# Performance work log

Hardware: AMD Instinct MI355X
Metric: run time of the kernel (lower is better)

Reference implementation:

```python
import jax, jax.numpy as jnp
import numpy as np

N_NODES = 50000
N_EDGES = 800000
N_GLOBALS = 64
DX, DE, DU = 128, 32, 32
HID, OUT = 128, 128
EPS = 1e-5


def _mlp(x, W1, b1, W2, b2, g, b):
    # Linear -> ReLU -> Linear -> ReLU (activate_final) -> LayerNorm (normalize)
    h = jax.nn.relu(x @ W1 + b1)
    h = jax.nn.relu(h @ W2 + b2)
    mu = jnp.mean(h, axis=-1, keepdims=True)
    var = jnp.var(h, axis=-1, keepdims=True)
    return g * (h - mu) * jax.lax.rsqrt(var + EPS) + b


def _mlp_params(key, d_in):
    k1, k2 = jax.random.split(key)
    W1 = jax.random.normal(k1, (d_in, HID), jnp.float32) / np.sqrt(d_in)
    b1 = jnp.zeros((HID,), jnp.float32)
    W2 = jax.random.normal(k2, (HID, OUT), jnp.float32) / np.sqrt(HID)
    b2 = jnp.zeros((OUT,), jnp.float32)
    g = jnp.ones((OUT,), jnp.float32)
    b = jnp.zeros((OUT,), jnp.float32)
    return W1, b1, W2, b2, g, b


def setup_inputs() -> dict:
    key = jax.random.key(0)
    ks = jax.random.split(key, 8)
    x = jax.random.normal(ks[0], (N_NODES, DX), jnp.float32)
    e = jax.random.normal(ks[1], (N_EDGES, DE), jnp.float32)
    u = jax.random.normal(ks[2], (N_GLOBALS, DU), jnp.float32)
    edge_index = jax.random.randint(ks[3], (2, N_EDGES), 0, N_NODES, jnp.int64 if jax.config.jax_enable_x64 else jnp.int32)
    batch = jnp.sort(jax.random.randint(ks[4], (N_NODES,), 0, N_GLOBALS))
    # edge MLP in: e(32) + recv(128) + send(128) + u(32) = 320
    eW1, eb1, eW2, eb2, eg, ebt = _mlp_params(ks[5], DE + DX + DX + DU)
    # node MLP in: x(128) + edge_aggr(128) + u(32) = 288
    nW1, nb1, nW2, nb2, ng, nbt = _mlp_params(ks[6], DX + OUT + DU)
    # global MLP in: u(32) + node_aggr(128) + edge_aggr(128) = 288
    gW1, gb1, gW2, gb2, gg, gbt = _mlp_params(ks[7], DU + OUT + OUT)
    return dict(x=x, e=e, u=u, edge_index=edge_index, batch=batch,
                eW1=eW1, eb1=eb1, eW2=eW2, eb2=eb2, eg=eg, ebt=ebt,
                nW1=nW1, nb1=nb1, nW2=nW2, nb2=nb2, ng=ng, nbt=nbt,
                gW1=gW1, gb1=gb1, gW2=gW2, gb2=gb2, gg=gg, gbt=gbt)


def reference(x, e, u, edge_index, batch,
              eW1, eb1, eW2, eb2, eg, ebt,
              nW1, nb1, nW2, nb2, ng, nbt,
              gW1, gb1, gW2, gb2, gg, gbt):
    row, col = edge_index[0], edge_index[1]
    edge_batch = batch[row]  # graph id per edge

    # --- EdgeModel: concat(edge, receiver, sender, global->edges) -> MLP ---
    edge_in = jnp.concatenate([e, x[col], x[row], u[edge_batch]], axis=1)
    e2 = _mlp(edge_in, eW1, eb1, eW2, eb2, eg, ebt)  # [N_EDGES, OUT]

    # --- NodeModel: concat(node, edges->node via receiver, global->nodes) -> MLP ---
    edge_to_node = jax.ops.segment_sum(e2, col, num_segments=N_NODES)
    node_in = jnp.concatenate([x, edge_to_node, u[batch]], axis=1)
    x2 = _mlp(node_in, nW1, nb1, nW2, nb2, ng, nbt)  # [N_NODES, OUT]

    # --- GlobalModel: concat(global, nodes->global, edges->global) -> MLP ---
    node_to_glob = jax.ops.segment_sum(x2, batch, num_segments=N_GLOBALS)
    edge_to_glob = jax.ops.segment_sum(e2, edge_batch, num_segments=N_GLOBALS)
    glob_in = jnp.concatenate([u, node_to_glob, edge_to_glob], axis=1)
    u2 = _mlp(glob_in, gW1, gb1, gW2, gb2, gg, gbt)  # [N_GLOBALS, OUT]

    return x2, e2, u2
```

## Files before the change

### kernel.cpp

```cpp
#include <hip/hip_runtime.h>
#include <hip/hip_bf16.h>

typedef __attribute__((ext_vector_type(8))) short bf16x8;
typedef __attribute__((ext_vector_type(4))) float f32x4;

#define EPSV 1e-5f
#define NN 50000
#define NE 800000
#define NG 64
#define SEGB 1000
#define MFMA16(a, b, c) __builtin_amdgcn_mfma_f32_16x16x32_bf16(a, b, c, 0, 0, 0)

__device__ __forceinline__ unsigned short f2bf(float f) {
  union { float f; unsigned u; } v; v.f = f;
  unsigned r = v.u + 0x7FFFu + ((v.u >> 16) & 1u);
  return (unsigned short)(r >> 16);
}
__device__ __forceinline__ float bf2f(unsigned short h) {
  union { unsigned u; float f; } v; v.u = ((unsigned)h) << 16;
  return v.f;
}


__global__ __launch_bounds__(256) void cvt_vec_kernel(
    const float* __restrict__ x, unsigned short* __restrict__ xb) {
  const int NX4 = (NN * 128) / 4;
  for (int idx = blockIdx.x * 256 + threadIdx.x; idx < NX4;
       idx += gridDim.x * 256) {
    float4 v = ((const float4*)x)[idx];
    ushort4 o;
    o.x = f2bf(v.x); o.y = f2bf(v.y); o.z = f2bf(v.z); o.w = f2bf(v.w);
    ((ushort4*)xb)[idx] = o;
  }
}

__global__ __launch_bounds__(256) void cvt_small_kernel(
    const float* __restrict__ u,
    const float* __restrict__ eW1, const float* __restrict__ eW2,
    const float* __restrict__ nW1, const float* __restrict__ nW2,
    unsigned short* __restrict__ ub,
    unsigned short* __restrict__ W1eT, unsigned short* __restrict__ WpqT,
    unsigned short* __restrict__ eW2T,
    unsigned short* __restrict__ nW1T, unsigned short* __restrict__ nW2T,
    float* __restrict__ Rg) {
  int i = blockIdx.x * 256 + threadIdx.x;
  const int R0 = NG * 32;
  const int R1 = R0 + 128 * 32;
  const int R2 = R1 + 256 * 128;
  const int R3 = R2 + 128 * 128;
  const int R4 = R3 + 128 * 320;
  const int R5 = R4 + 128 * 128;
  const int R6 = R5 + NG * 128;
  if (i < R0) {
    ub[i] = f2bf(u[i]);
  } else if (i < R1) {
    int j = i - R0; int n = j >> 5, k = j & 31;
    W1eT[j] = f2bf(eW1[k * 128 + n]);
  } else if (i < R2) {
    int j = i - R1; int n = j >> 7, k = j & 127;
    WpqT[j] = (n < 128) ? f2bf(eW1[(32 + k) * 128 + n])
                        : f2bf(eW1[(160 + k) * 128 + (n - 128)]);
  } else if (i < R3) {
    int j = i - R2; int n = j >> 7, k = j & 127;
    eW2T[j] = f2bf(eW2[k * 128 + n]);
  } else if (i < R4) {
    int j = i - R3; int n = j / 320, k = j % 320;
    nW1T[j] = (k < 288) ? f2bf(nW1[k * 128 + n]) : (unsigned short)0;
  } else if (i < R5) {
    int j = i - R4; int n = j >> 7, k = j & 127;
    nW2T[j] = f2bf(nW2[k * 128 + n]);
  } else if (i < R6) {
    int j = i - R5; int g = j >> 7, n = j & 127;
    float s = 0.f;
#pragma unroll
    for (int k = 0; k < 32; ++k) s += u[g * 32 + k] * eW1[(288 + k) * 128 + n];
    Rg[j] = s;
  }
}

__global__ __launch_bounds__(256, 2) void pq_kernel(
    const unsigned short* __restrict__ xb,
    const unsigned short* __restrict__ WpqT,
    unsigned short* __restrict__ PQ) {
  __shared__ __align__(16) unsigned short Asm[64][136];
  __shared__ __align__(16) unsigned short Bsm[256][72];
  const int tid = threadIdx.x;
  {
    const int r = tid >> 2, q = tid & 3;
    const int grow = blockIdx.x * 64 + r;
    const uint4 zero = {0u, 0u, 0u, 0u};
    if (grow < NN) {
      const uint4* xs = (const uint4*)(xb + (size_t)grow * 128 + q * 32);
#pragma unroll
      for (int k = 0; k < 4; ++k) *(uint4*)&Asm[r][q * 32 + k * 8] = xs[k];
    } else {
#pragma unroll
      for (int k = 0; k < 4; ++k) *(uint4*)&Asm[r][q * 32 + k * 8] = zero;
    }
  }
  const int w = tid >> 6, lane = tid & 63;
  const int l15 = lane & 15, lg = lane >> 4;
  f32x4 acc[16];
#pragma unroll
  for (int ni = 0; ni < 16; ++ni) acc[ni] = f32x4{0.f, 0.f, 0.f, 0.f};
  for (int kc = 0; kc < 2; ++kc) {
    {
      const uint4* src = (const uint4*)(WpqT + (size_t)tid * 128 + kc * 64);
#pragma unroll
      for (int k = 0; k < 8; ++k) *(uint4*)&Bsm[tid][k * 8] = src[k];
    }
    __syncthreads();
    bf16x8 a0 = *(bf16x8*)&Asm[w * 16 + l15][kc * 64 + lg * 8];
    bf16x8 a1 = *(bf16x8*)&Asm[w * 16 + l15][kc * 64 + 32 + lg * 8];
#pragma unroll
    for (int ni = 0; ni < 16; ++ni) {
      bf16x8 b0 = *(bf16x8*)&Bsm[ni * 16 + l15][lg * 8];
      bf16x8 b1 = *(bf16x8*)&Bsm[ni * 16 + l15][32 + lg * 8];
      acc[ni] = MFMA16(a0, b0, acc[ni]);
      acc[ni] = MFMA16(a1, b1, acc[ni]);
    }
    __syncthreads();
  }
  unsigned short (*Cl)[264] = (unsigned short(*)[264])&Bsm[0][0];
#pragma unroll
  for (int ni = 0; ni < 16; ++ni)
#pragma unroll
    for (int reg = 0; reg < 4; ++reg)
      Cl[w * 16 + lg * 4 + reg][l15 + ni * 16] = f2bf(acc[ni][reg]);
  __syncthreads();
  {
    const int r = tid >> 2, q = tid & 3;
    const int grow = blockIdx.x * 64 + r;
    if (grow < NN) {
#pragma unroll
      for (int k = 0; k < 8; ++k)
        *(uint4*)(PQ + (size_t)grow * 256 + q * 64 + k * 8) =
            *(uint4*)&Cl[r][q * 64 + k * 8];
    }
  }
}


__global__ __launch_bounds__(256) void pre_kernel(
    const int* __restrict__ rowIdx, const int* __restrict__ colIdx,
    int* __restrict__ cnt_r, int* __restrict__ cnt_s) {
  int i = blockIdx.x * 256 + threadIdx.x;
  if (i < NE) {
    atomicAdd(&cnt_r[colIdx[i]], 1);
    atomicAdd(&cnt_s[rowIdx[i]], 1);
  }
}

__global__ __launch_bounds__(1024) void scan2_kernel(
    const int* __restrict__ cnt_r, int* __restrict__ offs_r, int* __restrict__ cur_r,
    const int* __restrict__ cnt_s, int* __restrict__ offs_s, int* __restrict__ cur_s) {
  __shared__ int sums[1024];
  const int* cnt = blockIdx.x ? cnt_s : cnt_r;
  int* offs = blockIdx.x ? offs_s : offs_r;
  int* cur  = blockIdx.x ? cur_s : cur_r;
  const int t = threadIdx.x;
  const int base = t * 49;
  int s = 0;
  for (int j = 0; j < 49; ++j) {
    int idx = base + j;
    if (idx < NN) s += cnt[idx];
  }
  sums[t] = s;
  __syncthreads();
  for (int off = 1; off < 1024; off <<= 1) {
    int add = (t >= off) ? sums[t - off] : 0;
    __syncthreads();
    sums[t] += add;
    __syncthreads();
  }
  int run = (t == 0) ? 0 : sums[t - 1];
  for (int j = 0; j < 49; ++j) {
    int idx = base + j;
    if (idx < NN) {
      offs[idx] = run; cur[idx] = run;
      run += cnt[idx];
    }
  }
}

__global__ __launch_bounds__(256) void fill_both_kernel(
    const int* __restrict__ rowIdx, const int* __restrict__ colIdx,
    const int* __restrict__ batch,
    int* __restrict__ cur_r, int* __restrict__ cur_s,
    int* __restrict__ eidlist_r, int* __restrict__ eidlist_s,
    int* __restrict__ gs) {
  int i = blockIdx.x * 256 + threadIdx.x;
  if (i < NE) {
    const int c = colIdx[i];
    const int p = atomicAdd(&cur_r[c], 1);
    eidlist_r[p] = i;
    const int r = rowIdx[i];
    const int p2 = atomicAdd(&cur_s[r], 1);
    eidlist_s[p2] = i;
    gs[p2] = batch[r];
  }
}

__global__ __launch_bounds__(256, 3) void edge_kernel(
    const float* __restrict__ ef,
    const unsigned short* __restrict__ PQ,
    const float* __restrict__ Rg,
    const int* __restrict__ rowI, const int* __restrict__ colI,
    const int* __restrict__ batch,
    const unsigned short* __restrict__ W1eT,
    const unsigned short* __restrict__ W2T,
    const float* __restrict__ b1, const float* __restrict__ b2,
    const float* __restrict__ gam, const float* __restrict__ bet,
    float* __restrict__ outE) {
  __shared__ __align__(16) char U[27648];
  __shared__ __align__(16) unsigned short Hsm[64][136];
  __shared__ float cb1[128], cb2[128], cg[128], cbt[128];
  unsigned short (*B1e)[40] = (unsigned short(*)[40])U;
  unsigned short (*Ssm)[136] = (unsigned short(*)[136])(U + 10240);
  unsigned short (*Bsm)[72] = (unsigned short(*)[72])U;

  const int tid = threadIdx.x;
  const int base = blockIdx.x * 64;
  if (tid < 128) {
    cb1[tid] = b1[tid]; cb2[tid] = b2[tid];
    cg[tid] = gam[tid]; cbt[tid] = bet[tid];
    const uint4* s = (const uint4*)(W1eT + tid * 32);
#pragma unroll
    for (int k = 0; k < 4; ++k) *(uint4*)&B1e[tid][k * 8] = s[k];
  }

  {
    const int r = tid >> 2, q = tid & 3;
    const int grow = base + r;
    const int rcv = colI[grow];
    const int snd = rowI[grow];
    const int g = batch[snd];
    const unsigned short* pp = PQ + (size_t)rcv * 256 + q * 32;
    const unsigned short* qq = PQ + (size_t)snd * 256 + 128 + q * 32;
    const float* rr = Rg + g * 128 + q * 32;
#pragma unroll
    for (int k = 0; k < 8; ++k) {
      ushort4 pv = *(const ushort4*)(pp + k * 4);
      ushort4 qv = *(const ushort4*)(qq + k * 4);
      float4 rv = *(const float4*)(rr + k * 4);
      ushort4 o;
      o.x = f2bf(bf2f(pv.x) + bf2f(qv.x) + rv.x);
      o.y = f2bf(bf2f(pv.y) + bf2f(qv.y) + rv.y);
      o.z = f2bf(bf2f(pv.z) + bf2f(qv.z) + rv.z);
      o.w = f2bf(bf2f(pv.w) + bf2f(qv.w) + rv.w);
      *(ushort4*)&Ssm[r][q * 32 + k * 4] = o;
    }
  }
  __syncthreads();

  const int w = tid >> 6, lane = tid & 63;
  const int l15 = lane & 15, lg = lane >> 4;

  f32x4 acc[8];
#pragma unroll
  for (int ni = 0; ni < 8; ++ni) acc[ni] = f32x4{0.f, 0.f, 0.f, 0.f};
  {
    const int arow = base + w * 16 + l15;
    const float* ep = ef + (size_t)arow * 32 + lg * 8;
    float4 v0 = *(const float4*)ep;
    float4 v1 = *(const float4*)(ep + 4);
    bf16x8 a;
    a[0] = (short)f2bf(v0.x); a[1] = (short)f2bf(v0.y);
    a[2] = (short)f2bf(v0.z); a[3] = (short)f2bf(v0.w);
    a[4] = (short)f2bf(v1.x); a[5] = (short)f2bf(v1.y);
    a[6] = (short)f2bf(v1.z); a[7] = (short)f2bf(v1.w);
#pragma unroll
    for (int ni = 0; ni < 8; ++ni) {
      bf16x8 b0 = *(bf16x8*)&B1e[ni * 16 + l15][lg * 8];
      acc[ni] = MFMA16(a, b0, acc[ni]);
    }
  }

#pragma unroll
  for (int ni = 0; ni < 8; ++ni) {
    const int ncol = l15 + ni * 16;
    const float bias = cb1[ncol];
#pragma unroll
    for (int reg = 0; reg < 4; ++reg) {
      const int mrow = w * 16 + lg * 4 + reg;
      const float sv = bf2f(Ssm[mrow][ncol]);
      Hsm[mrow][ncol] = f2bf(fmaxf(acc[ni][reg] + sv + bias, 0.f));
    }
  }
  __syncthreads();

  f32x4 acc2[8];
#pragma unroll
  for (int ni = 0; ni < 8; ++ni) acc2[ni] = f32x4{0.f, 0.f, 0.f, 0.f};
  for (int kc = 0; kc < 2; ++kc) {
    {
      const int n = tid >> 1, half = tid & 1;
      const uint4* src = (const uint4*)(W2T + (size_t)n * 128 + kc * 64 + half * 32);
#pragma unroll
      for (int k = 0; k < 4; ++k)
        *(uint4*)&Bsm[n][half * 32 + k * 8] = src[k];
    }
    __syncthreads();
    bf16x8 a0 = *(bf16x8*)&Hsm[w * 16 + l15][kc * 64 + lg * 8];
    bf16x8 a1 = *(bf16x8*)&Hsm[w * 16 + l15][kc * 64 + 32 + lg * 8];
#pragma unroll
    for (int ni = 0; ni < 8; ++ni) {
      bf16x8 b0 = *(bf16x8*)&Bsm[ni * 16 + l15][lg * 8];
      bf16x8 b1 = *(bf16x8*)&Bsm[ni * 16 + l15][32 + lg * 8];
      acc2[ni] = MFMA16(a0, b0, acc2[ni]);
      acc2[ni] = MFMA16(a1, b1, acc2[ni]);
    }
    __syncthreads();
  }

  float hv[8][4];
  float sreg[4] = {0.f, 0.f, 0.f, 0.f}, ssreg[4] = {0.f, 0.f, 0.f, 0.f};
#pragma unroll
  for (int ni = 0; ni < 8; ++ni) {
    const int ncol = l15 + ni * 16;
    const float bias = cb2[ncol];
#pragma unroll
    for (int reg = 0; reg < 4; ++reg) {
      const float h = fmaxf(acc2[ni][reg] + bias, 0.f);
      hv[ni][reg] = h;
      sreg[reg] += h; ssreg[reg] += h * h;
    }
  }
#pragma unroll
  for (int reg = 0; reg < 4; ++reg) {
    float s = sreg[reg], ss = ssreg[reg];
#pragma unroll
    for (int off = 1; off < 16; off <<= 1) {
      s += __shfl_xor(s, off, 64);
      ss += __shfl_xor(ss, off, 64);
    }
    sreg[reg] = s; ssreg[reg] = ss;
  }
#pragma unroll
  for (int reg = 0; reg < 4; ++reg) {
    const int grow = base + w * 16 + lg * 4 + reg;
    const float mu = sreg[reg] * (1.f / 128.f);
    const float var = ssreg[reg] * (1.f / 128.f) - mu * mu;
    const float rstd = rsqrtf(var + EPSV);
#pragma unroll
    for (int ni = 0; ni < 8; ++ni) {
      const int ncol = l15 + ni * 16;
      const float y = cg[ncol] * (hv[ni][reg] - mu) * rstd + cbt[ncol];
      outE[(size_t)grow * 128 + ncol] = y;
    }
  }
}

__global__ __launch_bounds__(256, 3) void post_kernel(
    const float* __restrict__ outE,
    const int* __restrict__ eidl_s, const int* __restrict__ gsA,
    float* __restrict__ e2g,
    const unsigned short* __restrict__ xb,
    const unsigned short* __restrict__ ub,
    const int* __restrict__ batch,
    const int* __restrict__ offs, const int* __restrict__ cnt,
    const int* __restrict__ eidlist,
    const unsigned short* __restrict__ W1T,
    const unsigned short* __restrict__ W2T,
    const float* __restrict__ b1, const float* __restrict__ b2,
    const float* __restrict__ gam, const float* __restrict__ bet,
    float* __restrict__ outX, float* __restrict__ n2g) {
  __shared__ __align__(16) char U[33792];
  __shared__ __align__(16) unsigned short Usm[64][40];
  __shared__ __align__(16) unsigned short Bsm[128][40];
  __shared__ float cb1[128], cb2[128], cg[128], cbt[128];

  const int tid = threadIdx.x;

  if (blockIdx.x < SEGB) {
    const int c4 = (tid & 31) * 4;
    const int sub = tid >> 5;
    const int start = blockIdx.x * 800;
    int gcur = gsA[start + sub];
    float4 acc = {0.f, 0.f, 0.f, 0.f};
    for (int it = 0; it < 25; ++it) {
      const int pbase = start + sub + it * 32;
      int eid[4], g[4];
#pragma unroll
      for (int j = 0; j < 4; ++j) {
        eid[j] = eidl_s[pbase + j * 8];
        g[j]   = gsA[pbase + j * 8];
      }
      float4 v[4];
#pragma unroll
      for (int j = 0; j < 4; ++j)
        v[j] = *(const float4*)(outE + (size_t)eid[j] * 128 + c4);
#pragma unroll
      for (int j = 0; j < 4; ++j) {
        if (g[j] != gcur) {
          atomicAdd(&e2g[gcur * 128 + c4],     acc.x);
          atomicAdd(&e2g[gcur * 128 + c4 + 1], acc.y);
          atomicAdd(&e2g[gcur * 128 + c4 + 2], acc.z);
          atomicAdd(&e2g[gcur * 128 + c4 + 3], acc.w);
          gcur = g[j]; acc = float4{0.f, 0.f, 0.f, 0.f};
        }
        acc.x += v[j].x; acc.y += v[j].y; acc.z += v[j].z; acc.w += v[j].w;
      }
    }
    atomicAdd(&e2g[gcur * 128 + c4],     acc.x);
    atomicAdd(&e2g[gcur * 128 + c4 + 1], acc.y);
    atomicAdd(&e2g[gcur * 128 + c4 + 2], acc.z);
    atomicAdd(&e2g[gcur * 128 + c4 + 3], acc.w);
    return;
  }

  const int bx = blockIdx.x - SEGB;
  unsigned short (*Asm)[264] = (unsigned short(*)[264])U;
  unsigned short (*Hsm)[136] = (unsigned short(*)[136])U;
  float* bins = (float*)(U + 17408);

  if (tid < 128) {
    cb1[tid] = b1[tid]; cb2[tid] = b2[tid];
    cg[tid] = gam[tid]; cbt[tid] = bet[tid];
  }

  const int gmin = batch[bx * 64];
  const int gmax = batch[min(bx * 64 + 63, NN - 1)];
  const bool fastbins = (gmax - gmin) < 8;

  {
    const int r = tid >> 2, q = tid & 3;
    const int grow = bx * 64 + r;
    const bool valid = grow < NN;
    const uint4 zero = {0u, 0u, 0u, 0u};
    if (valid) {
      const uint4* xs = (const uint4*)(xb + (size_t)grow * 128 + q * 32);
#pragma unroll
      for (int k = 0; k < 4; ++k) *(uint4*)&Asm[r][q * 32 + k * 8] = xs[k];
    } else {
#pragma unroll
      for (int k = 0; k < 4; ++k) *(uint4*)&Asm[r][q * 32 + k * 8] = zero;
    }
    float4 a[8];
#pragma unroll
    for (int k = 0; k < 8; ++k) a[k] = float4{0.f, 0.f, 0.f, 0.f};
    if (valid) {
      const int start = offs[grow];
      const int deg = cnt[grow];
      int j = 0;
      for (; j + 2 <= deg; j += 2) {
        const int e0 = eidlist[start + j], e1 = eidlist[start + j + 1];
        const float4* s0 = (const float4*)(outE + (size_t)e0 * 128 + q * 32);
        const float4* s1 = (const float4*)(outE + (size_t)e1 * 128 + q * 32);
#pragma unroll
        for (int k = 0; k < 8; ++k) {
          float4 v0 = s0[k], v1 = s1[k];
          a[k].x += v0.x + v1.x; a[k].y += v0.y + v1.y;
          a[k].z += v0.z + v1.z; a[k].w += v0.w + v1.w;
        }
      }
      if (j < deg) {
        const int e0 = eidlist[start + j];
        const float4* s0 = (const float4*)(outE + (size_t)e0 * 128 + q * 32);
#pragma unroll
        for (int k = 0; k < 8; ++k) {
          float4 v0 = s0[k];
          a[k].x += v0.x; a[k].y += v0.y; a[k].z += v0.z; a[k].w += v0.w;
        }
      }
    }
#pragma unroll
    for (int k = 0; k < 8; ++k) {
      ushort4 o;
      o.x = f2bf(a[k].x); o.y = f2bf(a[k].y);
      o.z = f2bf(a[k].z); o.w = f2bf(a[k].w);
      *(ushort4*)&Asm[r][128 + q * 32 + k * 4] = o;
    }
    const int g = valid ? batch[grow] : 0;
    uint4 uv = valid ? *(const uint4*)(ub + g * 32 + q * 8) : zero;
    *(uint4*)&Usm[r][q * 8] = uv;
  }

  const int w = tid >> 6;
  const int lane = tid & 63;
  const int l15 = lane & 15, lg = lane >> 4;

  f32x4 acc[8];
#pragma unroll
  for (int ni = 0; ni < 8; ++ni) acc[ni] = f32x4{0.f, 0.f, 0.f, 0.f};

  for (int kc = 0; kc < 9; ++kc) {
    {
      const int n = tid >> 1, half = tid & 1;
      const uint4* src = (const uint4*)(W1T + (size_t)n * 320 + kc * 32 + half * 16);
      *(uint4*)&Bsm[n][half * 16] = src[0];
      *(uint4*)&Bsm[n][half * 16 + 8] = src[1];
    }
    __syncthreads();
    bf16x8 a0 = (kc < 8) ? *(bf16x8*)&Asm[w * 16 + l15][kc * 32 + lg * 8]
                         : *(bf16x8*)&Usm[w * 16 + l15][lg * 8];
#pragma unroll
    for (int ni = 0; ni < 8; ++ni) {
      bf16x8 bb = *(bf16x8*)&Bsm[ni * 16 + l15][lg * 8];
      acc[ni] = MFMA16(a0, bb, acc[ni]);
    }
    __syncthreads();
  }

#pragma unroll
  for (int ni = 0; ni < 8; ++ni) {
    const int ncol = l15 + ni * 16;
    const float bias = cb1[ncol];
#pragma unroll
    for (int reg = 0; reg < 4; ++reg) {
      const int mrow = w * 16 + lg * 4 + reg;
      Hsm[mrow][ncol] = f2bf(fmaxf(acc[ni][reg] + bias, 0.f));
    }
  }
  for (int i = tid; i < 8 * 128; i += 256) bins[i] = 0.f;

  f32x4 acc2[8];
#pragma unroll
  for (int ni = 0; ni < 8; ++ni) acc2[ni] = f32x4{0.f, 0.f, 0.f, 0.f};
  for (int kc = 0; kc < 4; ++kc) {
    {
      const int n = tid >> 1, half = tid & 1;
      const uint4* src = (const uint4*)(W2T + (size_t)n * 128 + kc * 32 + half * 16);
      *(uint4*)&Bsm[n][half * 16] = src[0];
      *(uint4*)&Bsm[n][half * 16 + 8] = src[1];
    }
    __syncthreads();
    bf16x8 a0 = *(bf16x8*)&Hsm[w * 16 + l15][kc * 32 + lg * 8];
#pragma unroll
    for (int ni = 0; ni < 8; ++ni) {
      bf16x8 bb = *(bf16x8*)&Bsm[ni * 16 + l15][lg * 8];
      acc2[ni] = MFMA16(a0, bb, acc2[ni]);
    }
    __syncthreads();
  }

  float hv[8][4];
  float sreg[4] = {0.f, 0.f, 0.f, 0.f}, ssreg[4] = {0.f, 0.f, 0.f, 0.f};
#pragma unroll
  for (int ni = 0; ni < 8; ++ni) {
    const int ncol = l15 + ni * 16;
    const float bias = cb2[ncol];
#pragma unroll
    for (int reg = 0; reg < 4; ++reg) {
      const float h = fmaxf(acc2[ni][reg] + bias, 0.f);
      hv[ni][reg] = h;
      sreg[reg] += h; ssreg[reg] += h * h;
    }
  }
#pragma unroll
  for (int reg = 0; reg < 4; ++reg) {
    float s = sreg[reg], ss = ssreg[reg];
#pragma unroll
    for (int off = 1; off < 16; off <<= 1) {
      s += __shfl_xor(s, off, 64);
      ss += __shfl_xor(ss, off, 64);
    }
    sreg[reg] = s; ssreg[reg] = ss;
  }
#pragma unroll
  for (int reg = 0; reg < 4; ++reg) {
    const int mrow = w * 16 + lg * 4 + reg;
    const int grow = bx * 64 + mrow;
    if (grow >= NN) continue;
    const float mu = sreg[reg] * (1.f / 128.f);
    const float var = ssreg[reg] * (1.f / 128.f) - mu * mu;
    const float rstd = rsqrtf(var + EPSV);
    const int g = batch[grow];
#pragma unroll
    for (int ni = 0; ni < 8; ++ni) {
      const int ncol = l15 + ni * 16;
      const float y = cg[ncol] * (hv[ni][reg] - mu) * rstd + cbt[ncol];
      outX[(size_t)grow * 128 + ncol] = y;
      if (fastbins) atomicAdd(&bins[(g - gmin) * 128 + ncol], y);
      else          atomicAdd(&n2g[g * 128 + ncol], y);
    }
  }
  if (fastbins) {
    __syncthreads();
    const int cntf = (gmax - gmin + 1) * 128;
    for (int i = tid; i < cntf; i += 256)
      atomicAdd(&n2g[gmin * 128 + i], bins[i]);
  }
}

__global__ __launch_bounds__(128) void glob_kernel(
    const float* __restrict__ u, const float* __restrict__ n2g,
    const float* __restrict__ e2g,
    const float* __restrict__ gW1, const float* __restrict__ gb1,
    const float* __restrict__ gW2, const float* __restrict__ gb2,
    const float* __restrict__ gg, const float* __restrict__ gbt,
    float* __restrict__ outU) {
  __shared__ float in[288];
  __shared__ float h1[128];
  __shared__ float red[4];
  const int g = blockIdx.x, t = threadIdx.x;
  if (t < 32) in[t] = u[g * 32 + t];
  in[32 + t] = n2g[g * 128 + t];
  in[160 + t] = e2g[g * 128 + t];
  __syncthreads();
  float a = gb1[t];
  for (int k = 0; k < 288; ++k) a += in[k] * gW1[k * 128 + t];
  h1[t] = fmaxf(a, 0.f);
  __syncthreads();
  float h = gb2[t];
  for (int k = 0; k < 128; ++k) h += h1[k] * gW2[k * 128 + t];
  h = fmaxf(h, 0.f);
  float s = h, ss = h * h;
  for (int off = 1; off < 64; off <<= 1) {
    s += __shfl_xor(s, off, 64);
    ss += __shfl_xor(ss, off, 64);
  }
  if ((t & 63) == 0) { red[(t >> 6) * 2] = s; red[(t >> 6) * 2 + 1] = ss; }
  __syncthreads();
  const float S = red[0] + red[2], SS = red[1] + red[3];
  const float mu = S * (1.f / 128.f);
  const float var = SS * (1.f / 128.f) - mu * mu;
  const float rstd = rsqrtf(var + EPSV);
  outU[g * 128 + t] = gg[t] * (h - mu) * rstd + gbt[t];
}

extern "C" void kernel_launch(void* const* d_in, const int* in_sizes, int n_in,
                              void* d_out, int out_size, void* d_ws,
                              size_t ws_size, hipStream_t stream) {
  const float* x   = (const float*)d_in[0];
  const float* e   = (const float*)d_in[1];
  const float* u   = (const float*)d_in[2];
  const int* eidx  = (const int*)d_in[3];
  const int* batch = (const int*)d_in[4];
  const float* eW1 = (const float*)d_in[5];
  const float* eb1 = (const float*)d_in[6];
  const float* eW2 = (const float*)d_in[7];
  const float* eb2 = (const float*)d_in[8];
  const float* eg  = (const float*)d_in[9];
  const float* ebt = (const float*)d_in[10];
  const float* nW1 = (const float*)d_in[11];
  const float* nb1 = (const float*)d_in[12];
  const float* nW2 = (const float*)d_in[13];
  const float* nb2 = (const float*)d_in[14];
  const float* ng  = (const float*)d_in[15];
  const float* nbt = (const float*)d_in[16];
  const float* gW1 = (const float*)d_in[17];
  const float* gb1 = (const float*)d_in[18];
  const float* gW2 = (const float*)d_in[19];
  const float* gb2 = (const float*)d_in[20];
  const float* gg  = (const float*)d_in[21];
  const float* gbt = (const float*)d_in[22];

  char* ws = (char*)d_ws;
  float* e2g           = (float*)(ws + 0);
  float* n2g           = (float*)(ws + 32768);
  int*   cnt_r         = (int*)  (ws + 65536);
  int*   cnt_s         = (int*)  (ws + 265536);
  int*   offs_r        = (int*)  (ws + 465536);
  int*   cur_r         = (int*)  (ws + 665536);
  int*   offs_s        = (int*)  (ws + 865536);
  int*   cur_s         = (int*)  (ws + 1065536);
  int*   eidlist_r     = (int*)  (ws + 1265536);
  int*   eidlist_s     = (int*)  (ws + 4465536);
  int*   gs            = (int*)  (ws + 7665536);
  unsigned short* xb   = (unsigned short*)(ws + 10865536);
  unsigned short* ub   = (unsigned short*)(ws + 23665536);
  unsigned short* W1eT = (unsigned short*)(ws + 23669632);
  unsigned short* WpqT = (unsigned short*)(ws + 23677824);
  unsigned short* eW2T = (unsigned short*)(ws + 23743360);
  unsigned short* nW1T = (unsigned short*)(ws + 23776128);
  unsigned short* nW2T = (unsigned short*)(ws + 23858048);
  unsigned short* PQ   = (unsigned short*)(ws + 23890816);
  float* Rg            = (float*)(ws + 49490816);

  hipMemsetAsync(ws, 0, 465536, stream);

  cvt_vec_kernel<<<1024, 256, 0, stream>>>(x, xb);
  cvt_small_kernel<<<472, 256, 0, stream>>>(u, eW1, eW2, nW1, nW2, ub, W1eT,
                                            WpqT, eW2T, nW1T, nW2T, Rg);
  pq_kernel<<<(NN + 63) / 64, 256, 0, stream>>>(xb, WpqT, PQ);

  float* outX = (float*)d_out;
  float* outE = outX + (size_t)NN * 128;
  float* outU = outE + (size_t)NE * 128;

  const int* rowI = eidx;
  const int* colI = eidx + NE;

  pre_kernel<<<(NE + 255) / 256, 256, 0, stream>>>(rowI, colI, cnt_r, cnt_s);
  scan2_kernel<<<2, 1024, 0, stream>>>(cnt_r, offs_r, cur_r,
                                       cnt_s, offs_s, cur_s);
  fill_both_kernel<<<(NE + 255) / 256, 256, 0, stream>>>(
      rowI, colI, batch, cur_r, cur_s, eidlist_r, eidlist_s, gs);

  edge_kernel<<<NE / 64, 256, 0, stream>>>(e, PQ, Rg, rowI, colI, batch,
                                           W1eT, eW2T, eb1, eb2, eg, ebt,
                                           outE);
  post_kernel<<<SEGB + (NN + 63) / 64, 256, 0, stream>>>(
      outE, eidlist_s, gs, e2g,
      xb, ub, batch, offs_r, cnt_r, eidlist_r,
      nW1T, nW2T, nb1, nb2, ng, nbt, outX, n2g);
  glob_kernel<<<NG, 128, 0, stream>>>(u, n2g, e2g, gW1, gb1, gW2, gb2, gg, gbt,
                                      outU);
}
```

Before: 842.4 us.

## Fuse edge-to-global segment sum into persistent edge kernel via shared-memory bins

Makes the edge kernel persistent over 512 blocks and accumulates each edge output row into per-block LDS bins indexed by graph id. The bins are written as per-block partials and summed by a small reduction kernel. This removes the sender-sorted CSR build (counting, scan and fill for senders) and the separate pass that re-read all of outE for the global aggregation. The cost is 128 LDS atomics per edge row, 32 KB of extra shared memory that lowers occupancy to 2 blocks per CU, and a 16 MB partial buffer plus its reduction.

```diff
diff --git a/kernel.cpp b/kernel.cpp
--- a/kernel.cpp
+++ b/kernel.cpp
@@ -8,7 +8,7 @@
 #define NN 50000
 #define NE 800000
 #define NG 64
-#define SEGB 1000
+#define EGRID 512
 #define MFMA16(a, b, c) __builtin_amdgcn_mfma_f32_16x16x32_bf16(a, b, c, 0, 0, 0)
 
 __device__ __forceinline__ unsigned short f2bf(float f) {
@@ -142,22 +142,15 @@
 
 
 __global__ __launch_bounds__(256) void pre_kernel(
-    const int* __restrict__ rowIdx, const int* __restrict__ colIdx,
-    int* __restrict__ cnt_r, int* __restrict__ cnt_s) {
+    const int* __restrict__ colIdx, int* __restrict__ cnt_r) {
   int i = blockIdx.x * 256 + threadIdx.x;
-  if (i < NE) {
-    atomicAdd(&cnt_r[colIdx[i]], 1);
-    atomicAdd(&cnt_s[rowIdx[i]], 1);
-  }
-}
-
-__global__ __launch_bounds__(1024) void scan2_kernel(
-    const int* __restrict__ cnt_r, int* __restrict__ offs_r, int* __restrict__ cur_r,
-    const int* __restrict__ cnt_s, int* __restrict__ offs_s, int* __restrict__ cur_s) {
+  if (i < NE) atomicAdd(&cnt_r[colIdx[i]], 1);
+}
+
+__global__ __launch_bounds__(1024) void scan_kernel(
+    const int* __restrict__ cnt, int* __restrict__ offs,
+    int* __restrict__ cur) {
   __shared__ int sums[1024];
-  const int* cnt = blockIdx.x ? cnt_s : cnt_r;
-  int* offs = blockIdx.x ? offs_s : offs_r;
-  int* cur  = blockIdx.x ? cur_s : cur_r;
   const int t = threadIdx.x;
   const int base = t * 49;
   int s = 0;
@@ -183,25 +176,17 @@
   }
 }
 
-__global__ __launch_bounds__(256) void fill_both_kernel(
-    const int* __restrict__ rowIdx, const int* __restrict__ colIdx,
-    const int* __restrict__ batch,
-    int* __restrict__ cur_r, int* __restrict__ cur_s,
-    int* __restrict__ eidlist_r, int* __restrict__ eidlist_s,
-    int* __restrict__ gs) {
+__global__ __launch_bounds__(256) void fill_kernel(
+    const int* __restrict__ colIdx, int* __restrict__ cur,
+    int* __restrict__ eidlist) {
   int i = blockIdx.x * 256 + threadIdx.x;
   if (i < NE) {
-    const int c = colIdx[i];
-    const int p = atomicAdd(&cur_r[c], 1);
-    eidlist_r[p] = i;
-    const int r = rowIdx[i];
-    const int p2 = atomicAdd(&cur_s[r], 1);
-    eidlist_s[p2] = i;
-    gs[p2] = batch[r];
-  }
-}
-
-__global__ __launch_bounds__(256, 3) void edge_kernel(
+    int p = atomicAdd(&cur[colIdx[i]], 1);
+    eidlist[p] = i;
+  }
+}
+
+__global__ __launch_bounds__(256, 2) void edge_kernel(
     const float* __restrict__ ef,
     const unsigned short* __restrict__ PQ,
     const float* __restrict__ Rg,
@@ -211,16 +196,15 @@
     const unsigned short* __restrict__ W2T,
     const float* __restrict__ b1, const float* __restrict__ b2,
     const float* __restrict__ gam, const float* __restrict__ bet,
-    float* __restrict__ outE) {
-  __shared__ __align__(16) char U[27648];
-  __shared__ __align__(16) unsigned short Hsm[64][136];
+    float* __restrict__ outE, float* __restrict__ e2g_part) {
+  __shared__ __align__(16) unsigned short B1e[128][40];
+  __shared__ __align__(16) unsigned short SH[64][136];
+  __shared__ __align__(16) unsigned short Bsm[128][72];
+  __shared__ float bins[NG * 128];
   __shared__ float cb1[128], cb2[128], cg[128], cbt[128];
-  unsigned short (*B1e)[40] = (unsigned short(*)[40])U;
-  unsigned short (*Ssm)[136] = (unsigned short(*)[136])(U + 10240);
-  unsigned short (*Bsm)[72] = (unsigned short(*)[72])U;
+  __shared__ int gsm[64];
 
   const int tid = threadIdx.x;
-  const int base = blockIdx.x * 64;
   if (tid < 128) {
     cb1[tid] = b1[tid]; cb2[tid] = b2[tid];
     cg[tid] = gam[tid]; cbt[tid] = bet[tid];
@@ -228,133 +212,153 @@
 #pragma unroll
     for (int k = 0; k < 4; ++k) *(uint4*)&B1e[tid][k * 8] = s[k];
   }
-
-  {
-    const int r = tid >> 2, q = tid & 3;
-    const int grow = base + r;
-    const int rcv = colI[grow];
-    const int snd = rowI[grow];
-    const int g = batch[snd];
-    const unsigned short* pp = PQ + (size_t)rcv * 256 + q * 32;
-    const unsigned short* qq = PQ + (size_t)snd * 256 + 128 + q * 32;
-    const float* rr = Rg + g * 128 + q * 32;
-#pragma unroll
-    for (int k = 0; k < 8; ++k) {
-      ushort4 pv = *(const ushort4*)(pp + k * 4);
-      ushort4 qv = *(const ushort4*)(qq + k * 4);
-      float4 rv = *(const float4*)(rr + k * 4);
-      ushort4 o;
-      o.x = f2bf(bf2f(pv.x) + bf2f(qv.x) + rv.x);
-      o.y = f2bf(bf2f(pv.y) + bf2f(qv.y) + rv.y);
-      o.z = f2bf(bf2f(pv.z) + bf2f(qv.z) + rv.z);
-      o.w = f2bf(bf2f(pv.w) + bf2f(qv.w) + rv.w);
-      *(ushort4*)&Ssm[r][q * 32 + k * 4] = o;
-    }
-  }
+  for (int i = tid; i < NG * 128; i += 256) bins[i] = 0.f;
   __syncthreads();
 
   const int w = tid >> 6, lane = tid & 63;
   const int l15 = lane & 15, lg = lane >> 4;
 
-  f32x4 acc[8];
-#pragma unroll
-  for (int ni = 0; ni < 8; ++ni) acc[ni] = f32x4{0.f, 0.f, 0.f, 0.f};
-  {
-    const int arow = base + w * 16 + l15;
-    const float* ep = ef + (size_t)arow * 32 + lg * 8;
-    float4 v0 = *(const float4*)ep;
-    float4 v1 = *(const float4*)(ep + 4);
-    bf16x8 a;
-    a[0] = (short)f2bf(v0.x); a[1] = (short)f2bf(v0.y);
-    a[2] = (short)f2bf(v0.z); a[3] = (short)f2bf(v0.w);
-    a[4] = (short)f2bf(v1.x); a[5] = (short)f2bf(v1.y);
-    a[6] = (short)f2bf(v1.z); a[7] = (short)f2bf(v1.w);
+  for (int tile = blockIdx.x; tile < NE / 64; tile += gridDim.x) {
+    const int base = tile * 64;
+
+    {
+      const int r = tid >> 2, q = tid & 3;
+      const int grow = base + r;
+      const int rcv = colI[grow];
+      const int snd = rowI[grow];
+      const int g = batch[snd];
+      if (q == 0) gsm[r] = g;
+      const unsigned short* pp = PQ + (size_t)rcv * 256 + q * 32;
+      const unsigned short* qq = PQ + (size_t)snd * 256 + 128 + q * 32;
+      const float* rr = Rg + g * 128 + q * 32;
+#pragma unroll
+      for (int k = 0; k < 8; ++k) {
+        ushort4 pv = *(const ushort4*)(pp + k * 4);
+        ushort4 qv = *(const ushort4*)(qq + k * 4);
+        float4 rv = *(const float4*)(rr + k * 4);
+        ushort4 o;
+        o.x = f2bf(bf2f(pv.x) + bf2f(qv.x) + rv.x);
+        o.y = f2bf(bf2f(pv.y) + bf2f(qv.y) + rv.y);
+        o.z = f2bf(bf2f(pv.z) + bf2f(qv.z) + rv.z);
+        o.w = f2bf(bf2f(pv.w) + bf2f(qv.w) + rv.w);
+        *(ushort4*)&SH[r][q * 32 + k * 4] = o;
+      }
+    }
+    __syncthreads();
+
+    f32x4 acc[8];
+#pragma unroll
+    for (int ni = 0; ni < 8; ++ni) acc[ni] = f32x4{0.f, 0.f, 0.f, 0.f};
+    {
+      const int arow = base + w * 16 + l15;
+      const float* ep = ef + (size_t)arow * 32 + lg * 8;
+      float4 v0 = *(const float4*)ep;
+      float4 v1 = *(const float4*)(ep + 4);
+      bf16x8 a;
+      a[0] = (short)f2bf(v0.x); a[1] = (short)f2bf(v0.y);
+      a[2] = (short)f2bf(v0.z); a[3] = (short)f2bf(v0.w);
+      a[4] = (short)f2bf(v1.x); a[5] = (short)f2bf(v1.y);
+      a[6] = (short)f2bf(v1.z); a[7] = (short)f2bf(v1.w);
+#pragma unroll
+      for (int ni = 0; ni < 8; ++ni) {
+        bf16x8 b0 = *(bf16x8*)&B1e[ni * 16 + l15][lg * 8];
+        acc[ni] = MFMA16(a, b0, acc[ni]);
+      }
+    }
+
 #pragma unroll
     for (int ni = 0; ni < 8; ++ni) {
-      bf16x8 b0 = *(bf16x8*)&B1e[ni * 16 + l15][lg * 8];
-      acc[ni] = MFMA16(a, b0, acc[ni]);
-    }
-  }
-
-#pragma unroll
-  for (int ni = 0; ni < 8; ++ni) {
-    const int ncol = l15 + ni * 16;
-    const float bias = cb1[ncol];
+      const int ncol = l15 + ni * 16;
+      const float bias = cb1[ncol];
+#pragma unroll
+      for (int reg = 0; reg < 4; ++reg) {
+        const int mrow = w * 16 + lg * 4 + reg;
+        const float sv = bf2f(SH[mrow][ncol]);
+        SH[mrow][ncol] = f2bf(fmaxf(acc[ni][reg] + sv + bias, 0.f));
+      }
+    }
+    __syncthreads();
+
+    f32x4 acc2[8];
+#pragma unroll
+    for (int ni = 0; ni < 8; ++ni) acc2[ni] = f32x4{0.f, 0.f, 0.f, 0.f};
+    for (int kc = 0; kc < 2; ++kc) {
+      {
+        const int n = tid >> 1, half = tid & 1;
+        const uint4* src = (const uint4*)(W2T + (size_t)n * 128 + kc * 64 + half * 32);
+#pragma unroll
+        for (int k = 0; k < 4; ++k)
+          *(uint4*)&Bsm[n][half * 32 + k * 8] = src[k];
+      }
+      __syncthreads();
+      bf16x8 a0 = *(bf16x8*)&SH[w * 16 + l15][kc * 64 + lg * 8];
+      bf16x8 a1 = *(bf16x8*)&SH[w * 16 + l15][kc * 64 + 32 + lg * 8];
+#pragma unroll
+      for (int ni = 0; ni < 8; ++ni) {
+        bf16x8 b0 = *(bf16x8*)&Bsm[ni * 16 + l15][lg * 8];
+        bf16x8 b1 = *(bf16x8*)&Bsm[ni * 16 + l15][32 + lg * 8];
+        acc2[ni] = MFMA16(a0, b0, acc2[ni]);
+        acc2[ni] = MFMA16(a1, b1, acc2[ni]);
+      }
+      __syncthreads();
+    }
+
+    float hv[8][4];
+    float sreg[4] = {0.f, 0.f, 0.f, 0.f}, ssreg[4] = {0.f, 0.f, 0.f, 0.f};
+#pragma unroll
+    for (int ni = 0; ni < 8; ++ni) {
+      const int ncol = l15 + ni * 16;
+      const float bias = cb2[ncol];
+#pragma unroll
+      for (int reg = 0; reg < 4; ++reg) {
+        const float h = fmaxf(acc2[ni][reg] + bias, 0.f);
+        hv[ni][reg] = h;
+        sreg[reg] += h; ssreg[reg] += h * h;
+      }
+    }
+#pragma unroll
+    for (int reg = 0; reg < 4; ++reg) {
+      float s = sreg[reg], ss = ssreg[reg];
+#pragma unroll
+      for (int off = 1; off < 16; off <<= 1) {
+        s += __shfl_xor(s, off, 64);
+        ss += __shfl_xor(ss, off, 64);
+      }
+      sreg[reg] = s; ssreg[reg] = ss;
+    }
 #pragma unroll
     for (int reg = 0; reg < 4; ++reg) {
       const int mrow = w * 16 + lg * 4 + reg;
-      const float sv = bf2f(Ssm[mrow][ncol]);
-      Hsm[mrow][ncol] = f2bf(fmaxf(acc[ni][reg] + sv + bias, 0.f));
-    }
-  }
-  __syncthreads();
-
-  f32x4 acc2[8];
-#pragma unroll
-  for (int ni = 0; ni < 8; ++ni) acc2[ni] = f32x4{0.f, 0.f, 0.f, 0.f};
-  for (int kc = 0; kc < 2; ++kc) {
-    {
-      const int n = tid >> 1, half = tid & 1;
-      const uint4* src = (const uint4*)(W2T + (size_t)n * 128 + kc * 64 + half * 32);
-#pragma unroll
-      for (int k = 0; k < 4; ++k)
-        *(uint4*)&Bsm[n][half * 32 + k * 8] = src[k];
-    }
-    __syncthreads();
-    bf16x8 a0 = *(bf16x8*)&Hsm[w * 16 + l15][kc * 64 + lg * 8];
-    bf16x8 a1 = *(bf16x8*)&Hsm[w * 16 + l15][kc * 64 + 32 + lg * 8];
-#pragma unroll
-    for (int ni = 0; ni < 8; ++ni) {
-      bf16x8 b0 = *(bf16x8*)&Bsm[ni * 16 + l15][lg * 8];
-      bf16x8 b1 = *(bf16x8*)&Bsm[ni * 16 + l15][32 + lg * 8];
-      acc2[ni] = MFMA16(a0, b0, acc2[ni]);
-      acc2[ni] = MFMA16(a1, b1, acc2[ni]);
-    }
-    __syncthreads();
-  }
-
-  float hv[8][4];
-  float sreg[4] = {0.f, 0.f, 0.f, 0.f}, ssreg[4] = {0.f, 0.f, 0.f, 0.f};
-#pragma unroll
-  for (int ni = 0; ni < 8; ++ni) {
-    const int ncol = l15 + ni * 16;
-    const float bias = cb2[ncol];
-#pragma unroll
-    for (int reg = 0; reg < 4; ++reg) {
-      const float h = fmaxf(acc2[ni][reg] + bias, 0.f);
-      hv[ni][reg] = h;
-      sreg[reg] += h; ssreg[reg] += h * h;
-    }
-  }
-#pragma unroll
-  for (int reg = 0; reg < 4; ++reg) {
-    float s = sreg[reg], ss = ssreg[reg];
-#pragma unroll
-    for (int off = 1; off < 16; off <<= 1) {
-      s += __shfl_xor(s, off, 64);
-      ss += __shfl_xor(ss, off, 64);
-    }
-    sreg[reg] = s; ssreg[reg] = ss;
-  }
-#pragma unroll
-  for (int reg = 0; reg < 4; ++reg) {
-    const int grow = base + w * 16 + lg * 4 + reg;
-    const float mu = sreg[reg] * (1.f / 128.f);
-    const float var = ssreg[reg] * (1.f / 128.f) - mu * mu;
-    const float rstd = rsqrtf(var + EPSV);
-#pragma unroll
-    for (int ni = 0; ni < 8; ++ni) {
-      const int ncol = l15 + ni * 16;
-      const float y = cg[ncol] * (hv[ni][reg] - mu) * rstd + cbt[ncol];
-      outE[(size_t)grow * 128 + ncol] = y;
-    }
-  }
-}
-
-__global__ __launch_bounds__(256, 3) void post_kernel(
+      const int grow = base + mrow;
+      const float mu = sreg[reg] * (1.f / 128.f);
+      const float var = ssreg[reg] * (1.f / 128.f) - mu * mu;
+      const float rstd = rsqrtf(var + EPSV);
+      const int gr = gsm[mrow];
+#pragma unroll
+      for (int ni = 0; ni < 8; ++ni) {
+        const int ncol = l15 + ni * 16;
+        const float y = cg[ncol] * (hv[ni][reg] - mu) * rstd + cbt[ncol];
+        outE[(size_t)grow * 128 + ncol] = y;
+        atomicAdd(&bins[gr * 128 + ncol], y);
+      }
+    }
+    __syncthreads();
+  }
+
+  float* dst = e2g_part + (size_t)blockIdx.x * (NG * 128);
+  for (int i = tid; i < NG * 128; i += 256) dst[i] = bins[i];
+}
+
+__global__ __launch_bounds__(256) void e2g_reduce_kernel(
+    const float* __restrict__ part, float* __restrict__ e2g) {
+  const int i = blockIdx.x * 256 + threadIdx.x;
+  float s = 0.f;
+  for (int p = 0; p < EGRID; ++p) s += part[(size_t)p * (NG * 128) + i];
+  e2g[i] = s;
+}
+
+__global__ __launch_bounds__(256, 3) void node_kernel(
     const float* __restrict__ outE,
-    const int* __restrict__ eidl_s, const int* __restrict__ gsA,
-    float* __restrict__ e2g,
     const unsigned short* __restrict__ xb,
     const unsigned short* __restrict__ ub,
     const int* __restrict__ batch,
@@ -371,45 +375,7 @@
   __shared__ float cb1[128], cb2[128], cg[128], cbt[128];
 
   const int tid = threadIdx.x;
-
-  if (blockIdx.x < SEGB) {
-    const int c4 = (tid & 31) * 4;
-    const int sub = tid >> 5;
-    const int start = blockIdx.x * 800;
-    int gcur = gsA[start + sub];
-    float4 acc = {0.f, 0.f, 0.f, 0.f};
-    for (int it = 0; it < 25; ++it) {
-      const int pbase = start + sub + it * 32;
-      int eid[4], g[4];
-#pragma unroll
-      for (int j = 0; j < 4; ++j) {
-        eid[j] = eidl_s[pbase + j * 8];
-        g[j]   = gsA[pbase + j * 8];
-      }
-      float4 v[4];
-#pragma unroll
-      for (int j = 0; j < 4; ++j)
-        v[j] = *(const float4*)(outE + (size_t)eid[j] * 128 + c4);
-#pragma unroll
-      for (int j = 0; j < 4; ++j) {
-        if (g[j] != gcur) {
-          atomicAdd(&e2g[gcur * 128 + c4],     acc.x);
-          atomicAdd(&e2g[gcur * 128 + c4 + 1], acc.y);
-          atomicAdd(&e2g[gcur * 128 + c4 + 2], acc.z);
-          atomicAdd(&e2g[gcur * 128 + c4 + 3], acc.w);
-          gcur = g[j]; acc = float4{0.f, 0.f, 0.f, 0.f};
-        }
-        acc.x += v[j].x; acc.y += v[j].y; acc.z += v[j].z; acc.w += v[j].w;
-      }
-    }
-    atomicAdd(&e2g[gcur * 128 + c4],     acc.x);
-    atomicAdd(&e2g[gcur * 128 + c4 + 1], acc.y);
-    atomicAdd(&e2g[gcur * 128 + c4 + 2], acc.z);
-    atomicAdd(&e2g[gcur * 128 + c4 + 3], acc.w);
-    return;
-  }
-
-  const int bx = blockIdx.x - SEGB;
+  const int bx = blockIdx.x;
   unsigned short (*Asm)[264] = (unsigned short(*)[264])U;
   unsigned short (*Hsm)[136] = (unsigned short(*)[136])U;
   float* bins = (float*)(U + 17408);
@@ -650,25 +616,21 @@
   float* e2g           = (float*)(ws + 0);
   float* n2g           = (float*)(ws + 32768);
   int*   cnt_r         = (int*)  (ws + 65536);
-  int*   cnt_s         = (int*)  (ws + 265536);
-  int*   offs_r        = (int*)  (ws + 465536);
-  int*   cur_r         = (int*)  (ws + 665536);
-  int*   offs_s        = (int*)  (ws + 865536);
-  int*   cur_s         = (int*)  (ws + 1065536);
-  int*   eidlist_r     = (int*)  (ws + 1265536);
-  int*   eidlist_s     = (int*)  (ws + 4465536);
-  int*   gs            = (int*)  (ws + 7665536);
-  unsigned short* xb   = (unsigned short*)(ws + 10865536);
-  unsigned short* ub   = (unsigned short*)(ws + 23665536);
-  unsigned short* W1eT = (unsigned short*)(ws + 23669632);
-  unsigned short* WpqT = (unsigned short*)(ws + 23677824);
-  unsigned short* eW2T = (unsigned short*)(ws + 23743360);
-  unsigned short* nW1T = (unsigned short*)(ws + 23776128);
-  unsigned short* nW2T = (unsigned short*)(ws + 23858048);
-  unsigned short* PQ   = (unsigned short*)(ws + 23890816);
-  float* Rg            = (float*)(ws + 49490816);
-
-  hipMemsetAsync(ws, 0, 465536, stream);
+  int*   offs_r        = (int*)  (ws + 265536);
+  int*   cur_r         = (int*)  (ws + 465536);
+  int*   eidlist_r     = (int*)  (ws + 665536);
+  float* e2g_part      = (float*)(ws + 3865536);
+  unsigned short* xb   = (unsigned short*)(ws + 20642752);
+  unsigned short* ub   = (unsigned short*)(ws + 33442752);
+  unsigned short* W1eT = (unsigned short*)(ws + 33446848);
+  unsigned short* WpqT = (unsigned short*)(ws + 33455040);
+  unsigned short* eW2T = (unsigned short*)(ws + 33520576);
+  unsigned short* nW1T = (unsigned short*)(ws + 33553344);
+  unsigned short* nW2T = (unsigned short*)(ws + 33635264);
+  unsigned short* PQ   = (unsigned short*)(ws + 33668032);
+  float* Rg            = (float*)(ws + 59268032);
+
+  hipMemsetAsync(ws, 0, 265536, stream);
 
   cvt_vec_kernel<<<1024, 256, 0, stream>>>(x, xb);
   cvt_small_kernel<<<472, 256, 0, stream>>>(u, eW1, eW2, nW1, nW2, ub, W1eT,
@@ -682,18 +644,16 @@
   const int* rowI = eidx;
   const int* colI = eidx + NE;
 
-  pre_kernel<<<(NE + 255) / 256, 256, 0, stream>>>(rowI, colI, cnt_r, cnt_s);
-  scan2_kernel<<<2, 1024, 0, stream>>>(cnt_r, offs_r, cur_r,
-                                       cnt_s, offs_s, cur_s);
-  fill_both_kernel<<<(NE + 255) / 256, 256, 0, stream>>>(
-      rowI, colI, batch, cur_r, cur_s, eidlist_r, eidlist_s, gs);
-
-  edge_kernel<<<NE / 64, 256, 0, stream>>>(e, PQ, Rg, rowI, colI, batch,
-                                           W1eT, eW2T, eb1, eb2, eg, ebt,
-                                           outE);
-  post_kernel<<<SEGB + (NN + 63) / 64, 256, 0, stream>>>(
-      outE, eidlist_s, gs, e2g,
-      xb, ub, batch, offs_r, cnt_r, eidlist_r,
+  pre_kernel<<<(NE + 255) / 256, 256, 0, stream>>>(colI, cnt_r);
+  scan_kernel<<<1, 1024, 0, stream>>>(cnt_r, offs_r, cur_r);
+  fill_kernel<<<(NE + 255) / 256, 256, 0, stream>>>(colI, cur_r, eidlist_r);
+
+  edge_kernel<<<EGRID, 256, 0, stream>>>(e, PQ, Rg, rowI, colI, batch,
+                                         W1eT, eW2T, eb1, eb2, eg, ebt,
+                                         outE, e2g_part);
+  e2g_reduce_kernel<<<32, 256, 0, stream>>>(e2g_part, e2g);
+  node_kernel<<<(NN + 63) / 64, 256, 0, stream>>>(
+      outE, xb, ub, batch, offs_r, cnt_r, eidlist_r,
       nW1T, nW2T, nb1, nb2, ng, nbt, outX, n2g);
   glob_kernel<<<NG, 128, 0, stream>>>(u, n2g, e2g, gW1, gb1, gW2, gb2, gg, gbt,
                                       outU);
```

Result: slower. 1.146 ms (+36.0%).
